# Kernel tuning notes

Measured on AMD Instinct MI355X. Metric: run time of the kernel, lower is better.

## Reference

```python
import jax, jax.numpy as jnp
import numpy as np

B, N, D, H = 4, 2048, 64, 8

def setup_inputs() -> dict:
    key = jax.random.key(0)
    ks = jax.random.split(key, 6)
    s = 0.05
    return {
        "x":  jax.random.normal(ks[0], (B, N, D), dtype=jnp.float32),
        "Wq": jax.random.normal(ks[1], (D, D * H), dtype=jnp.float32) * s,
        "Wk": jax.random.normal(ks[2], (D, D * H), dtype=jnp.float32) * s,
        "Wv": jax.random.normal(ks[3], (D, D * H), dtype=jnp.float32) * s,
        "Wu": jax.random.normal(ks[4], (D * H, D), dtype=jnp.float32) * s,
        "bu": jnp.zeros((D,), dtype=jnp.float32),
    }

def reference(x, Wq, Wk, Wv, Wu, bu):
    b, n, d = x.shape
    h = Wq.shape[1] // d
    # projections: each head has full width d (per the original module)
    q = (x @ Wq).reshape(b, n, h, d).transpose(0, 2, 1, 3)  # [b,h,n,d]
    k = (x @ Wk).reshape(b, n, h, d).transpose(0, 2, 1, 3)
    v = (x @ Wv).reshape(b, n, h, d).transpose(0, 2, 1, 3)
    scores = jnp.einsum('bhnd,bhmd->bhnm', q, k) / jnp.sqrt(jnp.float32(d))
    w = jax.nn.softmax(scores, axis=-1)
    y = jnp.einsum('bhnm,bhmd->bhnd', w, v)          # [b,h,n,d]
    y = y.transpose(0, 2, 1, 3).reshape(b, n, h * d)  # [b,n,h*d]
    return y @ Wu + bu
```

## Files before the change

### kernel.cpp

```cpp
#include <hip/hip_runtime.h>
#include <hip/hip_bf16.h>

#define BB 4
#define NN 2048
#define DD 64
#define HH 8
#define DHH 512

typedef __bf16 bf16_t;
typedef __bf16 bf16x8 __attribute__((ext_vector_type(8)));
typedef __bf16 bf16x4 __attribute__((ext_vector_type(4)));
typedef float f32x4 __attribute__((ext_vector_type(4)));

__device__ __forceinline__ void dma16(const void* g, void* l) {
    __builtin_amdgcn_global_load_lds(
        (const __attribute__((address_space(1))) unsigned int*)g,
        (__attribute__((address_space(3))) unsigned int*)l,
        16, 0, 0);
}

#define MFMA __builtin_amdgcn_mfma_f32_16x16x32_bf16

#define QSCALE 0.18033688011112042f

__global__ __launch_bounds__(256) void prep(
    const float* __restrict__ Wq, const float* __restrict__ Wk,
    const float* __restrict__ Wv, const float* __restrict__ Wu,
    bf16_t* __restrict__ Wqt, bf16_t* __restrict__ Wkt,
    bf16_t* __restrict__ Wvt, bf16_t* __restrict__ Wut)
{
    const int bid = blockIdx.x, tid = threadIdx.x;
    if (bid < 12) {
        const int m = bid >> 2, slice = bid & 3;
        const float* src = (m == 0) ? Wq : (m == 1) ? Wk : Wv;
        bf16_t* dst = (m == 0) ? Wqt : (m == 1) ? Wkt : Wvt;
        const float scale = (m == 0) ? QSCALE : 1.0f;
        const int dc = slice * 128 + (tid >> 1);
        const int kbase = (tid & 1) * 32;
        #pragma unroll
        for (int k0 = 0; k0 < 4; ++k0) {
            bf16x8 p;
            #pragma unroll
            for (int j = 0; j < 8; ++j)
                p[j] = (bf16_t)(src[(size_t)(kbase + k0 * 8 + j) * 512 + dc] * scale);
            *(bf16x8*)(dst + dc * 64 + kbase + k0 * 8) = p;
        }
    } else {
        const int kq = (bid - 12) * 128;
        const int dc = tid >> 2, sub = (tid & 3) * 32;
        #pragma unroll
        for (int k0 = 0; k0 < 4; ++k0) {
            bf16x8 p;
            #pragma unroll
            for (int j = 0; j < 8; ++j)
                p[j] = (bf16_t)Wu[(size_t)(kq + sub + k0 * 8 + j) * 64 + dc];
            *(bf16x8*)(Wut + dc * 512 + kq + sub + k0 * 8) = p;
        }
    }
}

__global__ __launch_bounds__(256) void qkv_mfma(
    const float* __restrict__ x, const bf16_t* __restrict__ Wqt,
    const bf16_t* __restrict__ Wkt, const bf16_t* __restrict__ Wvt,
    bf16_t* __restrict__ q, bf16_t* __restrict__ k, bf16_t* __restrict__ vt)
{
    const int n0   = blockIdx.x * 64;
    const int h    = blockIdx.y;
    const int tid  = threadIdx.x;
    const int w    = tid >> 6;
    const int lane = tid & 63;
    const int quad = lane >> 4;
    const int c    = lane & 15;
    const int cq   = c & 7;
    const int l8   = lane >> 3;
    const int lg   = (lane & 7) ^ l8;
    const int lo   = l8 * 128 + lg * 16;
    const int sw0  = ((quad    ) ^ cq) * 16;
    const int sw1  = ((quad + 4) ^ cq) * 16;
    const int w2048 = w * 2048;

    __shared__ __align__(16) float  xs[64 * 64];
    __shared__ __align__(16) bf16_t Wqs[64 * 64], Wks[64 * 64], Wvs[64 * 64];

    {
        const int rloc = lane >> 4;
        const int s    = lane & 15;
        #pragma unroll
        for (int j = 0; j < 4; ++j) {
            int chunk = w * 4 + j;
            int r7 = (chunk * 4 + rloc) & 7;
            const char* src = (const char*)(x + (size_t)(n0 + chunk * 4 + rloc) * 64)
                            + ((s & 8) | ((s & 7) ^ r7)) * 16;
            dma16(src, (char*)xs + chunk * 1024);
        }
    }
    const char* qg = (const char*)Wqt + (size_t)h * 8192;
    const char* kg = (const char*)Wkt + (size_t)h * 8192;
    const char* vg = (const char*)Wvt + (size_t)h * 8192;
    dma16(qg + w2048 + lo,        (char*)Wqs + w2048);
    dma16(qg + w2048 + 1024 + lo, (char*)Wqs + w2048 + 1024);
    dma16(kg + w2048 + lo,        (char*)Wks + w2048);
    dma16(kg + w2048 + 1024 + lo, (char*)Wks + w2048 + 1024);
    dma16(vg + w2048 + lo,        (char*)Wvs + w2048);
    dma16(vg + w2048 + 1024 + lo, (char*)Wvs + w2048 + 1024);
    __syncthreads();

    auto xfrag = [&](int row, int kk) -> bf16x8 {
        const char* rbase = (const char*)xs + row * 256;
        int g0 = kk * 8 + ((quad * 2    ) ^ cq);
        int g1 = kk * 8 + ((quad * 2 + 1) ^ cq);
        f32x4 a = *(const f32x4*)(rbase + g0 * 16);
        f32x4 b = *(const f32x4*)(rbase + g1 * 16);
        bf16x8 r;
        r[0] = (bf16_t)a[0]; r[1] = (bf16_t)a[1]; r[2] = (bf16_t)a[2]; r[3] = (bf16_t)a[3];
        r[4] = (bf16_t)b[0]; r[5] = (bf16_t)b[1]; r[6] = (bf16_t)b[2]; r[7] = (bf16_t)b[3];
        return r;
    };

    bf16x8 xf0 = xfrag(w * 16 + c, 0);
    bf16x8 xf1 = xfrag(w * 16 + c, 1);

    const int gr = n0 + w * 16 + c;
    const int bb = gr >> 11, nn = gr & 2047;
    bf16_t* qrow_g = q + (((size_t)bb * HH + h) * NN + nn) * DD;
    bf16_t* krow_g = k + (((size_t)bb * HH + h) * NN + nn) * DD;

    #pragma unroll
    for (int mb = 0; mb < 4; ++mb) {
        const char* aq = (const char*)Wqs + (mb * 16 + c) * 128;
        const char* ak = (const char*)Wks + (mb * 16 + c) * 128;
        f32x4 accq = (f32x4){0.f, 0.f, 0.f, 0.f};
        f32x4 acck = (f32x4){0.f, 0.f, 0.f, 0.f};
        accq = MFMA(*(const bf16x8*)(aq + sw0), xf0, accq, 0, 0, 0);
        accq = MFMA(*(const bf16x8*)(aq + sw1), xf1, accq, 0, 0, 0);
        acck = MFMA(*(const bf16x8*)(ak + sw0), xf0, acck, 0, 0, 0);
        acck = MFMA(*(const bf16x8*)(ak + sw1), xf1, acck, 0, 0, 0);
        bf16x4 pq = { (bf16_t)accq[0], (bf16_t)accq[1], (bf16_t)accq[2], (bf16_t)accq[3] };
        bf16x4 pk = { (bf16_t)acck[0], (bf16_t)acck[1], (bf16_t)acck[2], (bf16_t)acck[3] };
        *(bf16x4*)(qrow_g + mb * 16 + quad * 4) = pq;
        *(bf16x4*)(krow_g + mb * 16 + quad * 4) = pk;
    }

    const char* wvrow = (const char*)Wvs + (w * 16 + c) * 128;
    bf16x8 vf0 = *(const bf16x8*)(wvrow + sw0);
    bf16x8 vf1 = *(const bf16x8*)(wvrow + sw1);

    const int bb2 = n0 >> 11;
    bf16_t* vtrow_g = vt + (((size_t)bb2 * HH + h) * DD + (w * 16 + c)) * NN + (n0 & 2047);

    #pragma unroll
    for (int nb = 0; nb < 4; ++nb) {
        f32x4 acc = (f32x4){0.f, 0.f, 0.f, 0.f};
        acc = MFMA(xfrag(nb * 16 + c, 0), vf0, acc, 0, 0, 0);
        acc = MFMA(xfrag(nb * 16 + c, 1), vf1, acc, 0, 0, 0);
        bf16x4 p = { (bf16_t)acc[0], (bf16_t)acc[1], (bf16_t)acc[2], (bf16_t)acc[3] };
        *(bf16x4*)(vtrow_g + nb * 16 + quad * 4) = p;
    }
}

__global__ __launch_bounds__(256) void flash_attn(
    bf16_t* qy,
    const bf16_t* __restrict__ k, const bf16_t* __restrict__ vt)
{
    const int h    = blockIdx.x;
    const int n0   = blockIdx.y * 64;
    const int b    = blockIdx.z;
    const int tid  = threadIdx.x;
    const int w    = tid >> 6;
    const int lane = tid & 63;
    const int quad = lane >> 4;
    const int c    = lane & 15;
    const int cq   = c & 7;
    const int l8   = lane >> 3;
    const int lg   = (lane & 7) ^ l8;

    const int lo_k = l8 * 128  + lg * 16;
    const int lo_v = l8 * 4096 + lg * 16;

    const int sw0 = ((quad    ) ^ cq) * 16;
    const int sw1 = ((quad + 4) ^ cq) * 16;
    int pw[4];
    #pragma unroll
    for (int nb = 0; nb < 4; ++nb)
        pw[nb] = (((nb * 2 + (quad >> 1)) ^ cq) * 16) + (quad & 1) * 8;
    const int crow = c * 128;
    const int prow = (w * 16 + c) * 128;

    __shared__ __align__(16) bf16_t QPs[64 * 64];
    __shared__ __align__(16) bf16_t KVs[2][2][64 * 64];

    const size_t bh = (size_t)(b * HH + h);
    char* qp = (char*)(qy + bh * (size_t)(NN * DD));
    const char* kp = (const char*)(k  + bh * (size_t)(NN * DD));
    const char* vp = (const char*)(vt + bh * (size_t)(DD * NN));

    const int w2048 = w * 2048;

    const char* kptr  = kp + w2048 + lo_k;
    const char* vptr  = vp + w * 65536 + lo_v;
    const char* vptr2 = vptr + 32768;

    {
        const char* qg = qp + (size_t)(n0 + w * 16) * 128 + lo_k;
        char* ql = (char*)QPs + w2048;
        dma16(qg, ql); dma16(qg + 1024, ql + 1024);
    }
    {
        char* kl = (char*)&KVs[0][0][0] + w2048;
        char* vl = (char*)&KVs[0][1][0] + w2048;
        dma16(kptr, kl); dma16(kptr + 1024, kl + 1024);
        dma16(vptr, vl); dma16(vptr2, vl + 1024);
        kptr += 8192; vptr += 128; vptr2 += 128;
    }
    __syncthreads();

    bf16x8 qf0 = *(const bf16x8*)((const char*)QPs + prow + sw0);
    bf16x8 qf1 = *(const bf16x8*)((const char*)QPs + prow + sw1);

    float lsum = 0.f;
    f32x4 o[4];
    #pragma unroll
    for (int db = 0; db < 4; ++db) o[db] = (f32x4){0.f, 0.f, 0.f, 0.f};

    {
        char* kl = (char*)&KVs[1][0][0] + w2048;
        char* vl = (char*)&KVs[1][1][0] + w2048;
        dma16(kptr, kl); dma16(kptr + 1024, kl + 1024);
        dma16(vptr, vl); dma16(vptr2, vl + 1024);
        kptr += 8192; vptr += 128; vptr2 += 128;
    }

    char* pb = (char*)QPs;

    for (int kt = 0; kt < 32; ++kt) {
        const int buf = kt & 1;
        if (kt > 0) {
            __syncthreads();
            if (kt < 31) {
                char* kl = (char*)&KVs[buf ^ 1][0][0] + w2048;
                char* vl = (char*)&KVs[buf ^ 1][1][0] + w2048;
                dma16(kptr, kl); dma16(kptr + 1024, kl + 1024);
                dma16(vptr, vl); dma16(vptr2, vl + 1024);
                kptr += 8192; vptr += 128; vptr2 += 128;
            }
        }
        const char* kb = (const char*)&KVs[buf][0][0];
        const char* vb = (const char*)&KVs[buf][1][0];

        f32x4 s[4];
        #pragma unroll
        for (int nb = 0; nb < 4; ++nb) {
            s[nb] = (f32x4){0.f, 0.f, 0.f, 0.f};
            bf16x8 av0 = *(const bf16x8*)(kb + crow + nb * 2048 + sw0);
            bf16x8 av1 = *(const bf16x8*)(kb + crow + nb * 2048 + sw1);
            s[nb] = MFMA(av0, qf0, s[nb], 0, 0, 0);
            s[nb] = MFMA(av1, qf1, s[nb], 0, 0, 0);
        }

        #pragma unroll
        for (int nb = 0; nb < 4; ++nb) {
            float p0 = __builtin_amdgcn_exp2f(s[nb][0]);
            float p1 = __builtin_amdgcn_exp2f(s[nb][1]);
            float p2 = __builtin_amdgcn_exp2f(s[nb][2]);
            float p3 = __builtin_amdgcn_exp2f(s[nb][3]);
            lsum += (p0 + p1) + (p2 + p3);
            bf16x4 pk = { (bf16_t)p0, (bf16_t)p1, (bf16_t)p2, (bf16_t)p3 };
            *(bf16x4*)(pb + prow + pw[nb]) = pk;
        }

        bf16x8 pf0 = *(const bf16x8*)(pb + prow + sw0);
        bf16x8 pf1 = *(const bf16x8*)(pb + prow + sw1);

        #pragma unroll
        for (int db = 0; db < 4; ++db) {
            bf16x8 av0 = *(const bf16x8*)(vb + crow + db * 2048 + sw0);
            bf16x8 av1 = *(const bf16x8*)(vb + crow + db * 2048 + sw1);
            o[db] = MFMA(av0, pf0, o[db], 0, 0, 0);
            o[db] = MFMA(av1, pf1, o[db], 0, 0, 0);
        }
    }

    float l = lsum;
    l += __shfl_xor(l, 16, 64);
    l += __shfl_xor(l, 32, 64);
    float inv = 1.0f / l;

    #pragma unroll
    for (int db = 0; db < 4; ++db) {
        bf16x4 pk = { (bf16_t)(o[db][0] * inv), (bf16_t)(o[db][1] * inv),
                      (bf16_t)(o[db][2] * inv), (bf16_t)(o[db][3] * inv) };
        *(bf16x4*)(pb + prow + pw[db]) = pk;
    }
    __syncthreads();

    bf16_t* ypb = (bf16_t*)(qp + (size_t)n0 * 128);
    #pragma unroll
    for (int it = 0; it < 2; ++it) {
        int idx  = it * 256 + tid;
        int row  = idx >> 3;
        int gpos = idx & 7;
        int g    = gpos ^ (row & 7);
        bf16x8 val = *(const bf16x8*)((const char*)QPs + idx * 16);
        *(bf16x8*)(ypb + (size_t)row * DD + g * 8) = val;
    }
}

__global__ __launch_bounds__(256) void out_proj(
    const bf16_t* __restrict__ y,
    const bf16_t* __restrict__ Wut,
    const float* __restrict__ bu, float* __restrict__ out)
{
    const int rt   = blockIdx.x >> 1;
    const int dh   = blockIdx.x & 1;
    const int row0 = rt * 32;
    const int b    = row0 >> 11;
    const int nn0  = row0 & 2047;
    const int tid  = threadIdx.x;
    const int w    = tid >> 6;
    const int lane = tid & 63;
    const int quad = lane >> 4;
    const int c    = lane & 15;
    const int cq   = c & 7;

    __shared__ __align__(16) bf16_t ys[32 * 512];

    {
        const int hsel = lane >> 3;
        const int g7   = lane & 7;
        #pragma unroll
        for (int rr = 0; rr < 8; ++rr) {
            int row = w * 8 + rr;
            const char* src = (const char*)y
                + (((size_t)b * HH + hsel) * NN + nn0 + row) * 128
                + ((g7 ^ (row & 7)) * 16);
            dma16(src, (char*)ys + row * 1024);
        }
    }
    __syncthreads();

    const int rows16 = (w >> 1) * 16;
    const int mb     = dh * 2 + (w & 1);
    const char* yrow = (const char*)ys + (rows16 + c) * 1024;

    f32x4 acc = (f32x4){0.f, 0.f, 0.f, 0.f};
    #pragma unroll
    for (int kk = 0; kk < 16; ++kk) {
        int g = kk * 4 + quad;
        bf16x8 bfrag = *(const bf16x8*)(yrow + (((g & ~7) | ((g & 7) ^ cq)) * 16));
        bf16x8 afrag = *(const bf16x8*)((const char*)Wut
                        + (size_t)(mb * 16 + c) * 1024 + kk * 64 + quad * 16);
        acc = MFMA(afrag, bfrag, acc, 0, 0, 0);
    }

    float4 bb = *(const float4*)(bu + mb * 16 + quad * 4);
    float4 res = { acc[0] + bb.x, acc[1] + bb.y, acc[2] + bb.z, acc[3] + bb.w };
    float* op = out + (size_t)(row0 + rows16 + c) * DD + mb * 16 + quad * 4;
    *(float4*)op = res;
}

extern "C" void kernel_launch(void* const* d_in, const int* in_sizes, int n_in,
                              void* d_out, int out_size, void* d_ws, size_t ws_size,
                              hipStream_t stream) {
    const float* x  = (const float*)d_in[0];
    const float* Wq = (const float*)d_in[1];
    const float* Wk = (const float*)d_in[2];
    const float* Wv = (const float*)d_in[3];
    const float* Wu = (const float*)d_in[4];
    const float* bu = (const float*)d_in[5];
    float* out = (float*)d_out;

    const size_t SEG = (size_t)BB * HH * NN * DD * sizeof(bf16_t);
    char* ws = (char*)d_ws;
    bf16_t* qy  = (bf16_t*)(ws);
    bf16_t* k   = (bf16_t*)(ws + SEG);
    bf16_t* vt  = (bf16_t*)(ws + 2 * SEG);
    bf16_t* Wqt = (bf16_t*)(ws + 3 * SEG);
    bf16_t* Wkt = (bf16_t*)(ws + 3 * SEG + (1 << 16));
    bf16_t* Wvt = (bf16_t*)(ws + 3 * SEG + 2 * (1 << 16));
    bf16_t* Wut = (bf16_t*)(ws + 3 * SEG + 3 * (1 << 16));

    prep<<<dim3(16), dim3(256), 0, stream>>>(Wq, Wk, Wv, Wu, Wqt, Wkt, Wvt, Wut);
    qkv_mfma<<<dim3(128, 8), dim3(256), 0, stream>>>(x, Wqt, Wkt, Wvt, qy, k, vt);
    flash_attn<<<dim3(HH, NN / 64, BB), dim3(256), 0, stream>>>(qy, k, vt);
    out_proj<<<dim3(512), dim3(256), 0, stream>>>(qy, Wut, bu, out);
}
```

Baseline: 139.5 us.

## Load V fragments and Q directly from global, shrink LDS, drop out_proj staging

In flash_attn, the V^T tiles are no longer DMA'd into LDS. Each lane now reads its V MFMA operands straight from global memory every iteration, and Q fragments are loaded from global directly. This halves the K/V double buffer to K only and adds launch_bounds(256,4) to raise occupancy. out_proj drops its LDS staging and barrier and reads y fragments directly from global. The cost is more scattered global/L2 traffic and exposed load latency in the inner loop in exchange for less LDS, fewer barriers and higher occupancy.

```diff
diff --git a/kernel.cpp b/kernel.cpp
--- a/kernel.cpp
+++ b/kernel.cpp
@@ -158,7 +158,7 @@
     }
 }
 
-__global__ __launch_bounds__(256) void flash_attn(
+__global__ __launch_bounds__(256, 4) void flash_attn(
     bf16_t* qy,
     const bf16_t* __restrict__ k, const bf16_t* __restrict__ vt)
 {
@@ -174,8 +174,7 @@
     const int l8   = lane >> 3;
     const int lg   = (lane & 7) ^ l8;
 
-    const int lo_k = l8 * 128  + lg * 16;
-    const int lo_v = l8 * 4096 + lg * 16;
+    const int lo_k = l8 * 128 + lg * 16;
 
     const int sw0 = ((quad    ) ^ cq) * 16;
     const int sw1 = ((quad + 4) ^ cq) * 16;
@@ -186,8 +185,8 @@
     const int crow = c * 128;
     const int prow = (w * 16 + c) * 128;
 
-    __shared__ __align__(16) bf16_t QPs[64 * 64];
-    __shared__ __align__(16) bf16_t KVs[2][2][64 * 64];
+    __shared__ __align__(16) bf16_t Ps[64 * 64];
+    __shared__ __align__(16) bf16_t Ks[2][64 * 64];
 
     const size_t bh = (size_t)(b * HH + h);
     char* qp = (char*)(qy + bh * (size_t)(NN * DD));
@@ -195,57 +194,52 @@
     const char* vp = (const char*)(vt + bh * (size_t)(DD * NN));
 
     const int w2048 = w * 2048;
-
-    const char* kptr  = kp + w2048 + lo_k;
-    const char* vptr  = vp + w * 65536 + lo_v;
-    const char* vptr2 = vptr + 32768;
-
-    {
-        const char* qg = qp + (size_t)(n0 + w * 16) * 128 + lo_k;
-        char* ql = (char*)QPs + w2048;
-        dma16(qg, ql); dma16(qg + 1024, ql + 1024);
-    }
-    {
-        char* kl = (char*)&KVs[0][0][0] + w2048;
-        char* vl = (char*)&KVs[0][1][0] + w2048;
-        dma16(kptr, kl); dma16(kptr + 1024, kl + 1024);
-        dma16(vptr, vl); dma16(vptr2, vl + 1024);
-        kptr += 8192; vptr += 128; vptr2 += 128;
-    }
-    __syncthreads();
-
-    bf16x8 qf0 = *(const bf16x8*)((const char*)QPs + prow + sw0);
-    bf16x8 qf1 = *(const bf16x8*)((const char*)QPs + prow + sw1);
+    const char* kptr = kp + w2048 + lo_k;
+
+    dma16(kptr, (char*)Ks[0] + w2048);
+    dma16(kptr + 1024, (char*)Ks[0] + w2048 + 1024);
+    kptr += 8192;
+
+    const char* qrow = qp + (size_t)(n0 + w * 16 + c) * 128;
+    bf16x8 qf0 = *(const bf16x8*)(qrow + quad * 16);
+    bf16x8 qf1 = *(const bf16x8*)(qrow + 64 + quad * 16);
+
+    const char* vrow[4];
+    #pragma unroll
+    for (int db = 0; db < 4; ++db)
+        vrow[db] = vp + (size_t)(db * 16 + c) * 4096 + quad * 16;
 
     float lsum = 0.f;
     f32x4 o[4];
     #pragma unroll
     for (int db = 0; db < 4; ++db) o[db] = (f32x4){0.f, 0.f, 0.f, 0.f};
 
-    {
-        char* kl = (char*)&KVs[1][0][0] + w2048;
-        char* vl = (char*)&KVs[1][1][0] + w2048;
-        dma16(kptr, kl); dma16(kptr + 1024, kl + 1024);
-        dma16(vptr, vl); dma16(vptr2, vl + 1024);
-        kptr += 8192; vptr += 128; vptr2 += 128;
-    }
-
-    char* pb = (char*)QPs;
+    __syncthreads();
+
+    dma16(kptr, (char*)Ks[1] + w2048);
+    dma16(kptr + 1024, (char*)Ks[1] + w2048 + 1024);
+    kptr += 8192;
+
+    char* pb = (char*)Ps;
 
     for (int kt = 0; kt < 32; ++kt) {
         const int buf = kt & 1;
         if (kt > 0) {
             __syncthreads();
             if (kt < 31) {
-                char* kl = (char*)&KVs[buf ^ 1][0][0] + w2048;
-                char* vl = (char*)&KVs[buf ^ 1][1][0] + w2048;
-                dma16(kptr, kl); dma16(kptr + 1024, kl + 1024);
-                dma16(vptr, vl); dma16(vptr2, vl + 1024);
-                kptr += 8192; vptr += 128; vptr2 += 128;
+                dma16(kptr, (char*)Ks[buf ^ 1] + w2048);
+                dma16(kptr + 1024, (char*)Ks[buf ^ 1] + w2048 + 1024);
+                kptr += 8192;
             }
         }
-        const char* kb = (const char*)&KVs[buf][0][0];
-        const char* vb = (const char*)&KVs[buf][1][0];
+        const char* kb = (const char*)Ks[buf];
+
+        bf16x8 va[4][2];
+        #pragma unroll
+        for (int db = 0; db < 4; ++db) {
+            va[db][0] = *(const bf16x8*)(vrow[db] + (size_t)kt * 128);
+            va[db][1] = *(const bf16x8*)(vrow[db] + (size_t)kt * 128 + 64);
+        }
 
         f32x4 s[4];
         #pragma unroll
@@ -273,10 +267,8 @@
 
         #pragma unroll
         for (int db = 0; db < 4; ++db) {
-            bf16x8 av0 = *(const bf16x8*)(vb + crow + db * 2048 + sw0);
-            bf16x8 av1 = *(const bf16x8*)(vb + crow + db * 2048 + sw1);
-            o[db] = MFMA(av0, pf0, o[db], 0, 0, 0);
-            o[db] = MFMA(av1, pf1, o[db], 0, 0, 0);
+            o[db] = MFMA(va[db][0], pf0, o[db], 0, 0, 0);
+            o[db] = MFMA(va[db][1], pf1, o[db], 0, 0, 0);
         }
     }
 
@@ -300,7 +292,7 @@
         int row  = idx >> 3;
         int gpos = idx & 7;
         int g    = gpos ^ (row & 7);
-        bf16x8 val = *(const bf16x8*)((const char*)QPs + idx * 16);
+        bf16x8 val = *(const bf16x8*)((const char*)Ps + idx * 16);
         *(bf16x8*)(ypb + (size_t)row * DD + g * 8) = val;
     }
 }
@@ -320,42 +312,28 @@
     const int lane = tid & 63;
     const int quad = lane >> 4;
     const int c    = lane & 15;
-    const int cq   = c & 7;
-
-    __shared__ __align__(16) bf16_t ys[32 * 512];
-
-    {
-        const int hsel = lane >> 3;
-        const int g7   = lane & 7;
-        #pragma unroll
-        for (int rr = 0; rr < 8; ++rr) {
-            int row = w * 8 + rr;
-            const char* src = (const char*)y
-                + (((size_t)b * HH + hsel) * NN + nn0 + row) * 128
-                + ((g7 ^ (row & 7)) * 16);
-            dma16(src, (char*)ys + row * 1024);
-        }
-    }
-    __syncthreads();
 
     const int rows16 = (w >> 1) * 16;
     const int mb     = dh * 2 + (w & 1);
-    const char* yrow = (const char*)ys + (rows16 + c) * 1024;
+    const int n      = nn0 + rows16 + c;
+
+    const char* Wbase = (const char*)Wut + (size_t)(mb * 16 + c) * 1024;
+    const char* ybase = (const char*)y + (size_t)b * HH * NN * 128;
 
     f32x4 acc = (f32x4){0.f, 0.f, 0.f, 0.f};
     #pragma unroll
     for (int kk = 0; kk < 16; ++kk) {
         int g = kk * 4 + quad;
-        bf16x8 bfrag = *(const bf16x8*)(yrow + (((g & ~7) | ((g & 7) ^ cq)) * 16));
-        bf16x8 afrag = *(const bf16x8*)((const char*)Wut
-                        + (size_t)(mb * 16 + c) * 1024 + kk * 64 + quad * 16);
+        bf16x8 bfrag = *(const bf16x8*)(ybase
+                        + ((size_t)(g >> 3) * NN + n) * 128 + (g & 7) * 16);
+        bf16x8 afrag = *(const bf16x8*)(Wbase + kk * 64 + quad * 16);
         acc = MFMA(afrag, bfrag, acc, 0, 0, 0);
     }
 
     float4 bb = *(const float4*)(bu + mb * 16 + quad * 4);
-    float4 res = { acc[0] + bb.x, acc[1] + bb.y, acc[2] + bb.z, acc[3] + bb.w };
     float* op = out + (size_t)(row0 + rows16 + c) * DD + mb * 16 + quad * 4;
-    *(float4*)op = res;
+    *(float4*)op = (float4){ acc[0] + bb.x, acc[1] + bb.y,
+                             acc[2] + bb.z, acc[3] + bb.w };
 }
 
 extern "C" void kernel_launch(void* const* d_in, const int* in_sizes, int n_in,
```

After: 211.4 us. 51.5% more time.

## Store Q and K in FP8 and use FP8 MFMA for attention scores

Applied to the files above, without the earlier changes.

The QKV projection now writes Q and K as packed FP8 with a swizzled byte layout, and flash attention computes QK^T with the FP8 16x16x32 MFMA. Q fragments are loaded straight from global memory instead of staged through LDS, and K tiles in LDS are half the size. The output y moves to its own workspace buffer, and the attention kernel gets a launch-bounds occupancy hint. This halves K/Q traffic and LDS footprint, at the cost of lower precision in the softmax logits.

```diff
diff --git a/kernel.cpp b/kernel.cpp
--- a/kernel.cpp
+++ b/kernel.cpp
@@ -11,6 +11,8 @@
 typedef __bf16 bf16x8 __attribute__((ext_vector_type(8)));
 typedef __bf16 bf16x4 __attribute__((ext_vector_type(4)));
 typedef float f32x4 __attribute__((ext_vector_type(4)));
+typedef long long i64;
+typedef i64 i64x2 __attribute__((ext_vector_type(2)));
 
 __device__ __forceinline__ void dma16(const void* g, void* l) {
     __builtin_amdgcn_global_load_lds(
@@ -20,8 +22,10 @@
 }
 
 #define MFMA __builtin_amdgcn_mfma_f32_16x16x32_bf16
+#define MFMA8 __builtin_amdgcn_mfma_f32_16x16x32_fp8_fp8
 
 #define QSCALE 0.18033688011112042f
+
 
 __global__ __launch_bounds__(256) void prep(
     const float* __restrict__ Wq, const float* __restrict__ Wk,
@@ -62,7 +66,7 @@
 __global__ __launch_bounds__(256) void qkv_mfma(
     const float* __restrict__ x, const bf16_t* __restrict__ Wqt,
     const bf16_t* __restrict__ Wkt, const bf16_t* __restrict__ Wvt,
-    bf16_t* __restrict__ q, bf16_t* __restrict__ k, bf16_t* __restrict__ vt)
+    char* __restrict__ q8, char* __restrict__ k8, bf16_t* __restrict__ vt)
 {
     const int n0   = blockIdx.x * 64;
     const int h    = blockIdx.y;
@@ -122,8 +126,9 @@
 
     const int gr = n0 + w * 16 + c;
     const int bb = gr >> 11, nn = gr & 2047;
-    bf16_t* qrow_g = q + (((size_t)bb * HH + h) * NN + nn) * DD;
-    bf16_t* krow_g = k + (((size_t)bb * HH + h) * NN + nn) * DD;
+    char* qrow_g = q8 + (((size_t)bb * HH + h) * NN + nn) * 64;
+    char* krow_g = k8 + (((size_t)bb * HH + h) * NN + nn) * 64;
+    const int nsw = nn & 3;
 
     #pragma unroll
     for (int mb = 0; mb < 4; ++mb) {
@@ -135,10 +140,14 @@
         accq = MFMA(*(const bf16x8*)(aq + sw1), xf1, accq, 0, 0, 0);
         acck = MFMA(*(const bf16x8*)(ak + sw0), xf0, acck, 0, 0, 0);
         acck = MFMA(*(const bf16x8*)(ak + sw1), xf1, acck, 0, 0, 0);
-        bf16x4 pq = { (bf16_t)accq[0], (bf16_t)accq[1], (bf16_t)accq[2], (bf16_t)accq[3] };
-        bf16x4 pk = { (bf16_t)acck[0], (bf16_t)acck[1], (bf16_t)acck[2], (bf16_t)acck[3] };
-        *(bf16x4*)(qrow_g + mb * 16 + quad * 4) = pq;
-        *(bf16x4*)(krow_g + mb * 16 + quad * 4) = pk;
+        int g2  = (mb * 2 + (quad >> 1)) & 3;
+        int off = ((quad & 1) * 4) + ((mb >> 1) * 8) + ((g2 ^ nsw) * 16);
+        int pq = __builtin_amdgcn_cvt_pk_fp8_f32(accq[0], accq[1], 0, false);
+        pq     = __builtin_amdgcn_cvt_pk_fp8_f32(accq[2], accq[3], pq, true);
+        int pk = __builtin_amdgcn_cvt_pk_fp8_f32(acck[0], acck[1], 0, false);
+        pk     = __builtin_amdgcn_cvt_pk_fp8_f32(acck[2], acck[3], pk, true);
+        *(int*)(qrow_g + off) = pq;
+        *(int*)(krow_g + off) = pk;
     }
 
     const char* wvrow = (const char*)Wvs + (w * 16 + c) * 128;
@@ -158,9 +167,9 @@
     }
 }
 
-__global__ __launch_bounds__(256) void flash_attn(
-    bf16_t* qy,
-    const bf16_t* __restrict__ k, const bf16_t* __restrict__ vt)
+__global__ __launch_bounds__(256, 4) void flash_attn(
+    const char* __restrict__ q8, const char* __restrict__ k8,
+    const bf16_t* __restrict__ vt, bf16_t* __restrict__ y)
 {
     const int h    = blockIdx.x;
     const int n0   = blockIdx.y * 64;
@@ -174,8 +183,8 @@
     const int l8   = lane >> 3;
     const int lg   = (lane & 7) ^ l8;
 
-    const int lo_k = l8 * 128  + lg * 16;
     const int lo_v = l8 * 4096 + lg * 16;
+    const int ksw  = (quad ^ (c & 3)) * 16;
 
     const int sw0 = ((quad    ) ^ cq) * 16;
     const int sw1 = ((quad + 4) ^ cq) * 16;
@@ -186,75 +195,62 @@
     const int crow = c * 128;
     const int prow = (w * 16 + c) * 128;
 
-    __shared__ __align__(16) bf16_t QPs[64 * 64];
-    __shared__ __align__(16) bf16_t KVs[2][2][64 * 64];
+    __shared__ __align__(16) bf16_t Ps[64 * 64];
+    __shared__ __align__(16) char   Ks[2][4096];
+    __shared__ __align__(16) bf16_t Vs[2][64 * 64];
 
     const size_t bh = (size_t)(b * HH + h);
-    char* qp = (char*)(qy + bh * (size_t)(NN * DD));
-    const char* kp = (const char*)(k  + bh * (size_t)(NN * DD));
+    const char* qp = q8 + bh * (size_t)(NN * 64);
+    const char* kp = k8 + bh * (size_t)(NN * 64);
     const char* vp = (const char*)(vt + bh * (size_t)(DD * NN));
 
-    const int w2048 = w * 2048;
-
-    const char* kptr  = kp + w2048 + lo_k;
+    i64x2 qf = *(const i64x2*)(qp + (size_t)(n0 + w * 16 + c) * 64 + ksw);
+
+    const char* kptr  = kp + w * 1024 + lane * 16;
     const char* vptr  = vp + w * 65536 + lo_v;
     const char* vptr2 = vptr + 32768;
 
-    {
-        const char* qg = qp + (size_t)(n0 + w * 16) * 128 + lo_k;
-        char* ql = (char*)QPs + w2048;
-        dma16(qg, ql); dma16(qg + 1024, ql + 1024);
-    }
-    {
-        char* kl = (char*)&KVs[0][0][0] + w2048;
-        char* vl = (char*)&KVs[0][1][0] + w2048;
-        dma16(kptr, kl); dma16(kptr + 1024, kl + 1024);
-        dma16(vptr, vl); dma16(vptr2, vl + 1024);
-        kptr += 8192; vptr += 128; vptr2 += 128;
-    }
-    __syncthreads();
-
-    bf16x8 qf0 = *(const bf16x8*)((const char*)QPs + prow + sw0);
-    bf16x8 qf1 = *(const bf16x8*)((const char*)QPs + prow + sw1);
+    dma16(kptr,  (char*)Ks[0] + w * 1024);
+    dma16(vptr,  (char*)Vs[0] + w * 2048);
+    dma16(vptr2, (char*)Vs[0] + w * 2048 + 1024);
+    kptr += 4096; vptr += 128; vptr2 += 128;
 
     float lsum = 0.f;
     f32x4 o[4];
     #pragma unroll
     for (int db = 0; db < 4; ++db) o[db] = (f32x4){0.f, 0.f, 0.f, 0.f};
 
-    {
-        char* kl = (char*)&KVs[1][0][0] + w2048;
-        char* vl = (char*)&KVs[1][1][0] + w2048;
-        dma16(kptr, kl); dma16(kptr + 1024, kl + 1024);
-        dma16(vptr, vl); dma16(vptr2, vl + 1024);
-        kptr += 8192; vptr += 128; vptr2 += 128;
-    }
-
-    char* pb = (char*)QPs;
+    __syncthreads();
+
+    dma16(kptr,  (char*)Ks[1] + w * 1024);
+    dma16(vptr,  (char*)Vs[1] + w * 2048);
+    dma16(vptr2, (char*)Vs[1] + w * 2048 + 1024);
+    kptr += 4096; vptr += 128; vptr2 += 128;
+
+    char* pb = (char*)Ps;
 
     for (int kt = 0; kt < 32; ++kt) {
         const int buf = kt & 1;
         if (kt > 0) {
             __syncthreads();
             if (kt < 31) {
-                char* kl = (char*)&KVs[buf ^ 1][0][0] + w2048;
-                char* vl = (char*)&KVs[buf ^ 1][1][0] + w2048;
-                dma16(kptr, kl); dma16(kptr + 1024, kl + 1024);
-                dma16(vptr, vl); dma16(vptr2, vl + 1024);
-                kptr += 8192; vptr += 128; vptr2 += 128;
+                dma16(kptr,  (char*)Ks[buf ^ 1] + w * 1024);
+                dma16(vptr,  (char*)Vs[buf ^ 1] + w * 2048);
+                dma16(vptr2, (char*)Vs[buf ^ 1] + w * 2048 + 1024);
+                kptr += 4096; vptr += 128; vptr2 += 128;
             }
         }
-        const char* kb = (const char*)&KVs[buf][0][0];
-        const char* vb = (const char*)&KVs[buf][1][0];
+        const char* kb = (const char*)Ks[buf];
+        const char* vb = (const char*)Vs[buf];
 
         f32x4 s[4];
         #pragma unroll
         for (int nb = 0; nb < 4; ++nb) {
-            s[nb] = (f32x4){0.f, 0.f, 0.f, 0.f};
-            bf16x8 av0 = *(const bf16x8*)(kb + crow + nb * 2048 + sw0);
-            bf16x8 av1 = *(const bf16x8*)(kb + crow + nb * 2048 + sw1);
-            s[nb] = MFMA(av0, qf0, s[nb], 0, 0, 0);
-            s[nb] = MFMA(av1, qf1, s[nb], 0, 0, 0);
+            i64x2 av = *(const i64x2*)(kb + (nb * 16 + c) * 64 + ksw);
+            f32x4 t = (f32x4){0.f, 0.f, 0.f, 0.f};
+            t = MFMA8(av.x, qf.x, t, 0, 0, 0);
+            t = MFMA8(av.y, qf.y, t, 0, 0, 0);
+            s[nb] = t;
         }
 
         #pragma unroll
@@ -293,14 +289,14 @@
     }
     __syncthreads();
 
-    bf16_t* ypb = (bf16_t*)(qp + (size_t)n0 * 128);
+    bf16_t* ypb = y + bh * (size_t)(NN * DD) + (size_t)n0 * DD;
     #pragma unroll
     for (int it = 0; it < 2; ++it) {
         int idx  = it * 256 + tid;
         int row  = idx >> 3;
         int gpos = idx & 7;
         int g    = gpos ^ (row & 7);
-        bf16x8 val = *(const bf16x8*)((const char*)QPs + idx * 16);
+        bf16x8 val = *(const bf16x8*)((const char*)Ps + idx * 16);
         *(bf16x8*)(ypb + (size_t)row * DD + g * 8) = val;
     }
 }
@@ -369,18 +365,20 @@
     const float* bu = (const float*)d_in[5];
     float* out = (float*)d_out;
 
-    const size_t SEG = (size_t)BB * HH * NN * DD * sizeof(bf16_t);
+    const size_t SEG8 = (size_t)BB * HH * NN * 64;
+    const size_t SEG  = SEG8 * 2;
     char* ws = (char*)d_ws;
-    bf16_t* qy  = (bf16_t*)(ws);
-    bf16_t* k   = (bf16_t*)(ws + SEG);
-    bf16_t* vt  = (bf16_t*)(ws + 2 * SEG);
-    bf16_t* Wqt = (bf16_t*)(ws + 3 * SEG);
-    bf16_t* Wkt = (bf16_t*)(ws + 3 * SEG + (1 << 16));
-    bf16_t* Wvt = (bf16_t*)(ws + 3 * SEG + 2 * (1 << 16));
-    bf16_t* Wut = (bf16_t*)(ws + 3 * SEG + 3 * (1 << 16));
+    char*   q8  = ws;
+    char*   k8  = ws + SEG8;
+    bf16_t* vt  = (bf16_t*)(ws + 2 * SEG8);
+    bf16_t* y   = (bf16_t*)(ws + 2 * SEG8 + SEG);
+    bf16_t* Wqt = (bf16_t*)(ws + 2 * SEG8 + 2 * SEG);
+    bf16_t* Wkt = (bf16_t*)(ws + 2 * SEG8 + 2 * SEG + (1 << 16));
+    bf16_t* Wvt = (bf16_t*)(ws + 2 * SEG8 + 2 * SEG + 2 * (1 << 16));
+    bf16_t* Wut = (bf16_t*)(ws + 2 * SEG8 + 2 * SEG + 3 * (1 << 16));
 
     prep<<<dim3(16), dim3(256), 0, stream>>>(Wq, Wk, Wv, Wu, Wqt, Wkt, Wvt, Wut);
-    qkv_mfma<<<dim3(128, 8), dim3(256), 0, stream>>>(x, Wqt, Wkt, Wvt, qy, k, vt);
-    flash_attn<<<dim3(HH, NN / 64, BB), dim3(256), 0, stream>>>(qy, k, vt);
-    out_proj<<<dim3(512), dim3(256), 0, stream>>>(qy, Wut, bu, out);
-}
+    qkv_mfma<<<dim3(128, 8), dim3(256), 0, stream>>>(x, Wqt, Wkt, Wvt, q8, k8, vt);
+    flash_attn<<<dim3(HH, NN / 64, BB), dim3(256), 0, stream>>>(q8, k8, vt, y);
+    out_proj<<<dim3(512), dim3(256), 0, stream>>>(y, Wut, bu, out);
+}
```

After: 133.5 us. 1.04x faster.
